# Optimization experiments

Hardware: AMD Instinct MI355X
Metric: run time of the kernel (lower is better)

## Reference

```python
import jax, jax.numpy as jnp
import numpy as np

B, S, D_MODEL, D_K, D_V, H = 2, 2048, 1024, 1024, 1024, 16


def setup_inputs() -> dict:
    key = jax.random.key(0)
    ks = jax.random.split(key, 12)
    s = 0.02
    inp = {
        "queries": jax.random.normal(ks[0], (B, S, D_MODEL), jnp.float32),
        "keys": jax.random.normal(ks[1], (B, S, D_MODEL), jnp.float32),
        "values": jax.random.normal(ks[2], (B, S, D_MODEL), jnp.float32),
        # causal mask: 1 where attention is disallowed (added as -1e9*mask)
        "mask": jnp.triu(jnp.ones((1, 1, S, S), jnp.float32), k=1),
        "Wq": jax.random.normal(ks[3], (D_MODEL, D_K), jnp.float32) * s,
        "bq": jnp.zeros((D_K,), jnp.float32),
        "Wk": jax.random.normal(ks[4], (D_MODEL, D_K), jnp.float32) * s,
        "bk": jnp.zeros((D_K,), jnp.float32),
        "Wv": jax.random.normal(ks[5], (D_MODEL, D_V), jnp.float32) * s,
        "bv": jnp.zeros((D_V,), jnp.float32),
        "Wo": jax.random.normal(ks[6], (D_K, D_MODEL), jnp.float32) * s,
        "bo": jnp.zeros((D_MODEL,), jnp.float32),
    }
    return inp


def _split_heads(x):  # [B,S,D] -> [B,H,S,D/H]
    b, s, d = x.shape
    return x.reshape(b, s, H, d // H).transpose(0, 2, 1, 3)


def reference(queries, keys, values, mask, Wq, bq, Wk, bk, Wv, bv, Wo, bo):
    q = _split_heads(queries @ Wq + bq)   # [B,H,S,hd]
    k = _split_heads(keys @ Wk + bk)
    v = _split_heads(values @ Wv + bv)
    # NOTE: original scales by sqrt(full d_k), not per-head dim (faithful quirk)
    scores = jnp.einsum("bhqd,bhkd->bhqk", q, k) / jnp.sqrt(jnp.float32(D_K))
    scores = scores + (-1e9) * mask
    w = jax.nn.softmax(scores, axis=-1)
    out = jnp.einsum("bhqk,bhkd->bhqd", w, v)        # [B,H,S,hd]
    out = out.transpose(0, 2, 1, 3).reshape(q.shape[0], q.shape[2], D_K)
    return out @ Wo + bo
```

## Files before the change

### kernel.cpp

```cpp
#include <hip/hip_runtime.h>
#include <hip/hip_bf16.h>
#include <cstdint>

typedef __bf16 bf16;
typedef __bf16 bf16x2 __attribute__((ext_vector_type(2)));
typedef __bf16 bf16x4 __attribute__((ext_vector_type(4)));
typedef __bf16 bf16x8 __attribute__((ext_vector_type(8)));
typedef float f32x4 __attribute__((ext_vector_type(4)));
typedef float f32x16 __attribute__((ext_vector_type(16)));
typedef unsigned int u32;

#define B_ 2
#define S_ 2048
#define DM 1024
#define H_ 16
#define HD 64

__device__ __forceinline__ void gload_lds16(const bf16* g, bf16* l) {
  __builtin_amdgcn_global_load_lds((const __attribute__((address_space(1))) void*)g,
                                   (__attribute__((address_space(3))) void*)l,
                                   16, 0, 0);
}

__device__ __forceinline__ u32 cvt_pk_bf16(float lo, float hi) {
  u32 r;
  asm("v_cvt_pk_bf16_f32 %0, %1, %2" : "=v"(r) : "v"(lo), "v"(hi));
  return r;
}

__device__ __forceinline__ bf16x8 cvt8(f32x4 lo, f32x4 hi) {
  bf16x8 o;
#pragma unroll
  for (int j = 0; j < 4; j++) { o[j] = (bf16)lo[j]; o[j + 4] = (bf16)hi[j]; }
  return o;
}

__global__ __launch_bounds__(256) void transposeW_k(
    const float* __restrict__ w0, const float* __restrict__ w1,
    const float* __restrict__ w2, const float* __restrict__ w3,
    bf16* __restrict__ t0, bf16* __restrict__ t1,
    bf16* __restrict__ t2, bf16* __restrict__ t3) {
  const float* src = (blockIdx.z == 0) ? w0 : (blockIdx.z == 1) ? w1
                     : (blockIdx.z == 2) ? w2 : w3;
  bf16* dst = (blockIdx.z == 0) ? t0 : (blockIdx.z == 1) ? t1
              : (blockIdx.z == 2) ? t2 : t3;
  __shared__ float tile[32][33];
  const int tx = threadIdx.x, ty = threadIdx.y;
  const int x0 = blockIdx.x * 32, y0 = blockIdx.y * 32;
#pragma unroll
  for (int r = 0; r < 4; r++)
    tile[ty + r * 8][tx] = src[(size_t)(y0 + ty + r * 8) * DM + x0 + tx];
  __syncthreads();
#pragma unroll
  for (int r = 0; r < 4; r++)
    dst[(size_t)(x0 + ty + r * 8) * DM + y0 + tx] = (bf16)tile[tx][ty + r * 8];
}

struct GArgs { const void* A; const bf16* Bt; const float* bias; void* C; };
struct GArgs3 { GArgs g[3]; };

__global__ __launch_bounds__(512, 1) void gemm128_k(GArgs3 args, int M, int N,
                                                    int K) {
  __shared__ __align__(16) bf16 SA_[73728];
  bf16* const SB_ = SA_ + 24576;

  const int nwg = gridDim.x;
  const int id = blockIdx.x;
  const int wgid = (id & 7) * (nwg >> 3) + (id >> 3);
  const int z = wgid >> 7;
  const int rem = wgid & 127;
  const int tx = rem & 3, ty = rem >> 2;
  const GArgs ga = args.g[z];
  const int m0 = ty * 128, n0 = tx * 256;

  const int tid = threadIdx.x;
  const int lane = tid & 63, w = tid >> 6;
  const int l15 = lane & 15, q = lane >> 4;
  const int wr = w >> 2, wc = w & 3;

  const float* gAf[2];
  int dAwr[2];
#pragma unroll
  for (int i = 0; i < 2; i++) {
    const int ci = i * 512 + w * 64 + lane;
    const int row = ci >> 3, sc = (ci & 7) ^ (row & 7);
    gAf[i] = (const float*)ga.A + (size_t)(m0 + row) * K + sc * 8;
    dAwr[i] = ci * 8;
  }
  const bf16* gB[4];
  int dB[4];
#pragma unroll
  for (int i = 0; i < 4; i++) {
    const int ci = i * 512 + w * 64 + lane;
    const int row = ci >> 3, sc = (ci & 7) ^ (row & 7);
    gB[i] = ga.Bt + (size_t)(n0 + row) * K + sc * 8;
    dB[i] = (i * 512 + w * 64) * 8;
  }

  const int cA0 = (q ^ (l15 & 7)) * 8;
  const int cA1 = ((4 + q) ^ (l15 & 7)) * 8;

  f32x4 acc[4][4] = {};
  const int NT = K >> 6;

  f32x4 a0l = *(const f32x4*)(gAf[0]);
  f32x4 a0h = *(const f32x4*)(gAf[0] + 4);
  f32x4 a1l = *(const f32x4*)(gAf[1]);
  f32x4 a1h = *(const f32x4*)(gAf[1] + 4);
  f32x4 c0l = *(const f32x4*)(gAf[0] + 64);
  f32x4 c0h = *(const f32x4*)(gAf[0] + 68);
  f32x4 c1l = *(const f32x4*)(gAf[1] + 64);
  f32x4 c1h = *(const f32x4*)(gAf[1] + 68);
#pragma unroll
  for (int i = 0; i < 4; i++) gload_lds16(gB[i], SB_ + dB[i]);
  f32x4 p0l = *(const f32x4*)(gAf[0] + 128);
  f32x4 p0h = *(const f32x4*)(gAf[0] + 132);
  f32x4 p1l = *(const f32x4*)(gAf[1] + 128);
  f32x4 p1h = *(const f32x4*)(gAf[1] + 132);
#pragma unroll
  for (int i = 0; i < 4; i++) gload_lds16(gB[i] + 64, SB_ + 16384 + dB[i]);
  *(bf16x8*)(SA_ + dAwr[0]) = cvt8(a0l, a0h);
  *(bf16x8*)(SA_ + dAwr[1]) = cvt8(a1l, a1h);
  *(bf16x8*)(SA_ + 8192 + dAwr[0]) = cvt8(c0l, c0h);
  *(bf16x8*)(SA_ + 8192 + dAwr[1]) = cvt8(c1l, c1h);
  asm volatile("s_waitcnt vmcnt(8) lgkmcnt(0)" ::: "memory");
  __builtin_amdgcn_s_barrier();

  for (int t = 0; t < NT; ++t) {
    const int rb = t % 3;
    const int w2 = (t + 2) % 3;
    *(bf16x8*)(SA_ + w2 * 8192 + dAwr[0]) = cvt8(p0l, p0h);
    *(bf16x8*)(SA_ + w2 * 8192 + dAwr[1]) = cvt8(p1l, p1h);
    const int ka = ((t + 3 < NT) ? t + 3 : NT - 1) << 6;
    p0l = *(const f32x4*)(gAf[0] + ka); p0h = *(const f32x4*)(gAf[0] + ka + 4);
    p1l = *(const f32x4*)(gAf[1] + ka); p1h = *(const f32x4*)(gAf[1] + ka + 4);
    const int kb2 = ((t + 2 < NT) ? t + 2 : NT - 1) << 6;
#pragma unroll
    for (int i = 0; i < 4; i++)
      gload_lds16(gB[i] + kb2, SB_ + w2 * 16384 + dB[i]);

    const bf16* Ab = SA_ + rb * 8192;
    const bf16* Bb = SB_ + rb * 16384;
    bf16x8 a[4][2], b[4][2];
#pragma unroll
    for (int mt = 0; mt < 4; mt++) {
      const int ro = (wr * 64 + mt * 16 + l15) * 64;
      a[mt][0] = *(const bf16x8*)(Ab + ro + cA0);
      a[mt][1] = *(const bf16x8*)(Ab + ro + cA1);
    }
#pragma unroll
    for (int nt = 0; nt < 4; nt++) {
      const int ro = (wc * 64 + nt * 16 + l15) * 64;
      b[nt][0] = *(const bf16x8*)(Bb + ro + cA0);
      b[nt][1] = *(const bf16x8*)(Bb + ro + cA1);
    }
    __builtin_amdgcn_s_setprio(1);
#pragma unroll
    for (int mt = 0; mt < 4; mt++)
#pragma unroll
      for (int nt = 0; nt < 4; nt++)
#pragma unroll
        for (int kk = 0; kk < 2; kk++)
          acc[mt][nt] = __builtin_amdgcn_mfma_f32_16x16x32_bf16(
              a[mt][kk], b[nt][kk], acc[mt][nt], 0, 0, 0);
    __builtin_amdgcn_s_setprio(0);

    asm volatile("s_waitcnt vmcnt(8) lgkmcnt(0)" ::: "memory");
    __builtin_amdgcn_s_barrier();
  }

  asm volatile("s_waitcnt vmcnt(0) lgkmcnt(0)" ::: "memory");
  __builtin_amdgcn_s_barrier();

  bf16* Ws = SA_ + w * 4352;
#pragma unroll
  for (int nt = 0; nt < 4; nt++) {
    const float bv = ga.bias[n0 + wc * 64 + nt * 16 + l15];
#pragma unroll
    for (int mt = 0; mt < 4; mt++)
#pragma unroll
      for (int r = 0; r < 4; r++)
        Ws[(mt * 16 + q * 4 + r) * 68 + nt * 16 + l15] =
            (bf16)(acc[mt][nt][r] + bv);
  }
#pragma unroll
  for (int p = 0; p < 8; p++) {
    const int lr = p * 8 + (lane >> 3), c0 = (lane & 7) * 8;
    bf16x4 lo = *(const bf16x4*)(Ws + lr * 68 + c0);
    bf16x4 hi = *(const bf16x4*)(Ws + lr * 68 + c0 + 4);
    bf16x8 o;
#pragma unroll
    for (int j = 0; j < 4; j++) { o[j] = lo[j]; o[j + 4] = hi[j]; }
    *(bf16x8*)((bf16*)ga.C + (size_t)(m0 + wr * 64 + lr) * N + n0 + wc * 64 + c0) = o;
  }
}

__global__ __launch_bounds__(512, 1) void gemmo_k(const bf16* __restrict__ A,
                                                  const bf16* __restrict__ Bt,
                                                  const float* __restrict__ bias,
                                                  float* __restrict__ C,
                                                  int M, int N, int K) {
  __shared__ __align__(16) bf16 SA_[49152];
  bf16* const SB_ = SA_ + 24576;

  const int id = blockIdx.x;
  const int wgid = (id & 7) * 32 + (id >> 3);
  const int tx = wgid & 7, ty = wgid >> 3;
  const int m0 = ty * 128, n0 = tx * 128;

  const int tid = threadIdx.x;
  const int lane = tid & 63, w = tid >> 6;
  const int l15 = lane & 15, q = lane >> 4;
  const int wr = w >> 2, wc = w & 3;

  const bf16* gA[2];
  const bf16* gB[2];
  int dd[2];
#pragma unroll
  for (int i = 0; i < 2; i++) {
    const int ci = i * 512 + w * 64 + lane;
    const int row = ci >> 3, sc = (ci & 7) ^ (row & 7);
    gA[i] = A + (size_t)(m0 + row) * K + sc * 8;
    gB[i] = Bt + (size_t)(n0 + row) * K + sc * 8;
    dd[i] = ci * 8;
  }

  const int cA0 = (q ^ (l15 & 7)) * 8;
  const int cA1 = ((4 + q) ^ (l15 & 7)) * 8;

  f32x4 acc[4][2] = {};
  const int NT = K >> 6;

#pragma unroll
  for (int tt = 0; tt < 2; tt++) {
    const int k0 = tt * 64;
    gload_lds16(gA[0] + k0, SA_ + tt * 8192 + dd[0]);
    gload_lds16(gA[1] + k0, SA_ + tt * 8192 + dd[1]);
    gload_lds16(gB[0] + k0, SB_ + tt * 8192 + dd[0]);
    gload_lds16(gB[1] + k0, SB_ + tt * 8192 + dd[1]);
  }
  asm volatile("s_waitcnt vmcnt(4)" ::: "memory");
  __builtin_amdgcn_s_barrier();

  for (int t = 0; t < NT; ++t) {
    const int rb = t % 3;
    const int wb = (t + 2) % 3;
    const int kpre = ((t + 2 < NT) ? t + 2 : NT - 1) << 6;
    gload_lds16(gA[0] + kpre, SA_ + wb * 8192 + dd[0]);
    gload_lds16(gA[1] + kpre, SA_ + wb * 8192 + dd[1]);
    gload_lds16(gB[0] + kpre, SB_ + wb * 8192 + dd[0]);
    gload_lds16(gB[1] + kpre, SB_ + wb * 8192 + dd[1]);

    const bf16* Ab = SA_ + rb * 8192;
    const bf16* Bb = SB_ + rb * 8192;
    bf16x8 a[4][2], b[2][2];
#pragma unroll
    for (int mt = 0; mt < 4; mt++) {
      const int ro = (wr * 64 + mt * 16 + l15) * 64;
      a[mt][0] = *(const bf16x8*)(Ab + ro + cA0);
      a[mt][1] = *(const bf16x8*)(Ab + ro + cA1);
    }
#pragma unroll
    for (int nt = 0; nt < 2; nt++) {
      const int ro = (wc * 32 + nt * 16 + l15) * 64;
      b[nt][0] = *(const bf16x8*)(Bb + ro + cA0);
      b[nt][1] = *(const bf16x8*)(Bb + ro + cA1);
    }

    __builtin_amdgcn_s_setprio(1);
#pragma unroll
    for (int mt = 0; mt < 4; mt++)
#pragma unroll
      for (int nt = 0; nt < 2; nt++)
#pragma unroll
        for (int kk = 0; kk < 2; kk++)
          acc[mt][nt] = __builtin_amdgcn_mfma_f32_16x16x32_bf16(
              a[mt][kk], b[nt][kk], acc[mt][nt], 0, 0, 0);
    __builtin_amdgcn_s_setprio(0);

    asm volatile("s_waitcnt vmcnt(4)" ::: "memory");
    __builtin_amdgcn_s_barrier();
  }

  asm volatile("s_waitcnt vmcnt(0)" ::: "memory");
  __builtin_amdgcn_s_barrier();

  float* Ws = (float*)SA_ + w * 2304;
#pragma unroll
  for (int nt = 0; nt < 2; nt++) {
    const float bv = bias[n0 + wc * 32 + nt * 16 + l15];
#pragma unroll
    for (int mt = 0; mt < 4; mt++)
#pragma unroll
      for (int r = 0; r < 4; r++)
        Ws[(mt * 16 + q * 4 + r) * 36 + nt * 16 + l15] = acc[mt][nt][r] + bv;
  }
#pragma unroll
  for (int p = 0; p < 8; p++) {
    const int lr = p * 8 + (lane >> 3), c0 = (lane & 7) * 4;
    f32x4 v = *(const f32x4*)(Ws + lr * 36 + c0);
    *(f32x4*)(C + (size_t)(m0 + wr * 64 + lr) * N + n0 + wc * 32 + c0) = v;
  }
}

__global__ __launch_bounds__(512, 4) void attn_k(const bf16* __restrict__ Qp,
                                                 const bf16* __restrict__ Kp,
                                                 const bf16* __restrict__ Vp,
                                                 bf16* __restrict__ Op) {
  const int g = blockIdx.x;
  const int xcd = g & 7, s = g >> 3;
  const int gl = s & 3, tau = s >> 2;
  const int bh = xcd * 4 + gl;
  const int b = bh >> 4, h = bh & 15;
  const int xt = (tau < 8) ? tau : 23 - tau;
  const int i0 = xt * 128;
  const int NI = 2 * xt + 2;

  const int tid = threadIdx.x;
  const int lane = tid & 63, w = tid >> 6;
  const int l31 = lane & 31, hi = lane >> 5;
  const int qq = w >> 1, kh = w & 1;

  __shared__ __align__(16) char smem[33792];
  bf16 (*Ks)[64][64] = (bf16 (*)[64][64])smem;
  bf16 (*Vts)[64][64] = (bf16 (*)[64][64])(smem + 16384);

  const size_t headoff = (size_t)b * S_ * DM + h * HD;
  const bf16* Kb = Kp + headoff;
  const bf16* Vb = Vp + headoff;

  const int kr = tid >> 3, kcb = (tid & 7) * 8;
  const int cK = ((tid & 7) ^ (kr & 7)) * 8;
  const int d0 = (tid & 31) * 2, kq = (tid >> 5) * 4;
  const int cV0 = ((kq >> 3) ^ (d0 & 7)) * 8 + (kq & 7);
  const int cV1 = ((kq >> 3) ^ ((d0 + 1) & 7)) * 8 + (kq & 7);
  const float QSCALE = 0.04508422f;

  bf16x8 qreg[4];
  {
    const bf16* qb = Qp + headoff + (size_t)(i0 + qq * 32 + l31) * DM + hi * 8;
#pragma unroll
    for (int kk = 0; kk < 4; kk++) {
      bf16x8 v = *(const bf16x8*)(qb + kk * 16);
      bf16x8 o;
#pragma unroll
      for (int j = 0; j < 8; j++) o[j] = (bf16)((float)v[j] * QSCALE);
      qreg[kk] = o;
    }
  }

  bf16x8 kR = *(const bf16x8*)(Kb + (size_t)kr * DM + kcb);
  bf16x2 vR[4];
#pragma unroll
  for (int j = 0; j < 4; j++)
    vR[j] = *(const bf16x2*)(Vb + (size_t)(kq + j) * DM + d0);
  *(bf16x8*)&Ks[0][kr][cK] = kR;
  {
    bf16x4 vlo, vhi;
#pragma unroll
    for (int j = 0; j < 4; j++) { vlo[j] = vR[j][0]; vhi[j] = vR[j][1]; }
    *(bf16x4*)&Vts[0][d0][cV0] = vlo;
    *(bf16x4*)&Vts[0][d0 + 1][cV1] = vhi;
  }
  kR = *(const bf16x8*)(Kb + (size_t)(64 + kr) * DM + kcb);
#pragma unroll
  for (int j = 0; j < 4; j++)
    vR[j] = *(const bf16x2*)(Vb + (size_t)(64 + kq + j) * DM + d0);
  __syncthreads();

  f32x16 oacc0 = {}, oacc1 = {};
  float rsum = 0.f;
  int buf = 0;
  const int qbase = i0 + qq * 32;

  for (int t = 0; t < NI; ++t, buf ^= 1) {
    if (t + 1 < NI) {
      *(bf16x8*)&Ks[buf ^ 1][kr][cK] = kR;
      bf16x4 vlo, vhi;
#pragma unroll
      for (int j = 0; j < 4; j++) { vlo[j] = vR[j][0]; vhi[j] = vR[j][1]; }
      *(bf16x4*)&Vts[buf ^ 1][d0][cV0] = vlo;
      *(bf16x4*)&Vts[buf ^ 1][d0 + 1][cV1] = vhi;
    }
    if (t + 2 < NI) {
      const size_t jn = (size_t)(t + 2) * 64;
      kR = *(const bf16x8*)(Kb + (jn + kr) * DM + kcb);
#pragma unroll
      for (int j = 0; j < 4; j++)
        vR[j] = *(const bf16x2*)(Vb + (jn + kq + j) * DM + d0);
    }

    const int kbase = t * 64 + kh * 32;
    if (kbase <= qbase + 31) {
      f32x16 sa = {}, sb = {};
      __builtin_amdgcn_s_setprio(1);
#pragma unroll
      for (int kk = 0; kk < 2; kk++) {
        bf16x8 ka = *(const bf16x8*)
            &Ks[buf][kh * 32 + l31][((2 * kk + hi) ^ (l31 & 7)) * 8];
        sa = __builtin_amdgcn_mfma_f32_32x32x16_bf16(ka, qreg[kk], sa, 0, 0, 0);
      }
#pragma unroll
      for (int kk = 2; kk < 4; kk++) {
        bf16x8 ka = *(const bf16x8*)
            &Ks[buf][kh * 32 + l31][((2 * kk + hi) ^ (l31 & 7)) * 8];
        sb = __builtin_amdgcn_mfma_f32_32x32x16_bf16(ka, qreg[kk], sb, 0, 0, 0);
      }
      __builtin_amdgcn_s_setprio(0);

      float p[16];
      if (kbase + 31 > qbase) {
        const int qrl = qbase + l31;
#pragma unroll
        for (int r = 0; r < 16; r++) {
          const int keyl = kbase + (r & 3) + 8 * (r >> 2) + 4 * hi;
          p[r] = (keyl <= qrl) ? __builtin_amdgcn_exp2f(sa[r] + sb[r]) : 0.f;
        }
      } else {
#pragma unroll
        for (int r = 0; r < 16; r++)
          p[r] = __builtin_amdgcn_exp2f(sa[r] + sb[r]);
      }
      {
        float q0 = (p[0] + p[1]) + (p[2] + p[3]);
        float q1 = (p[4] + p[5]) + (p[6] + p[7]);
        float q2 = (p[8] + p[9]) + (p[10] + p[11]);
        float q3 = (p[12] + p[13]) + (p[14] + p[15]);
        rsum += (q0 + q1) + (q2 + q3);
      }

      u32 Aq[4][2];
#pragma unroll
      for (int t2 = 0; t2 < 4; t2++) {
        Aq[t2][0] = cvt_pk_bf16(p[4 * t2 + 0], p[4 * t2 + 1]);
        Aq[t2][1] = cvt_pk_bf16(p[4 * t2 + 2], p[4 * t2 + 3]);
      }
      bf16x8 pb[2];
#pragma unroll
      for (int s2 = 0; s2 < 2; s2++) {
        auto e0 = __builtin_amdgcn_permlane32_swap(Aq[2 * s2][0], Aq[2 * s2 + 1][0], false, false);
        auto e1 = __builtin_amdgcn_permlane32_swap(Aq[2 * s2][1], Aq[2 * s2 + 1][1], false, false);
        union { u32 u[4]; bf16x8 v; } cv;
        cv.u[0] = e0[0]; cv.u[1] = e1[0]; cv.u[2] = e0[1]; cv.u[3] = e1[1];
        pb[s2] = cv.v;
      }

      __builtin_amdgcn_s_setprio(1);
#pragma unroll
      for (int s2 = 0; s2 < 2; s2++) {
        const int cv = ((kh * 4 + s2 * 2 + hi) ^ (l31 & 7)) * 8;
        bf16x8 va0 = *(const bf16x8*)&Vts[buf][l31][cv];
        bf16x8 va1 = *(const bf16x8*)&Vts[buf][32 + l31][cv];
        oacc0 = __builtin_amdgcn_mfma_f32_32x32x16_bf16(va0, pb[s2], oacc0, 0, 0, 0);
        oacc1 = __builtin_amdgcn_mfma_f32_32x32x16_bf16(va1, pb[s2], oacc1, 0, 0, 0);
      }
      __builtin_amdgcn_s_setprio(0);
    }

    __syncthreads();
  }

  float rtot_w = rsum + __shfl_xor(rsum, 32);
  float* osum = (float*)smem;
  float* auxf = (float*)(smem + 32768);
  if (kh == 0) {
#pragma unroll
    for (int m = 0; m < 2; m++)
#pragma unroll
      for (int rq = 0; rq < 4; rq++) {
        f32x4 v4;
#pragma unroll
        for (int e = 0; e < 4; e++)
          v4[e] = m ? oacc1[rq * 4 + e] : oacc0[rq * 4 + e];
        *(f32x4*)(osum + qq * 2048 + (m * 4 + rq) * 256 + lane * 4) = v4;
      }
  }
  if (lane < 32) auxf[w * 32 + lane] = rtot_w;
  __syncthreads();
  if (kh == 1) {
#pragma unroll
    for (int m = 0; m < 2; m++)
#pragma unroll
      for (int rq = 0; rq < 4; rq++) {
        float* pp = osum + qq * 2048 + (m * 4 + rq) * 256 + lane * 4;
        f32x4 v4 = *(f32x4*)pp;
#pragma unroll
        for (int e = 0; e < 4; e++)
          v4[e] += m ? oacc1[rq * 4 + e] : oacc0[rq * 4 + e];
        *(f32x4*)pp = v4;
      }
  }
  __syncthreads();

  {
    const int q = tid >> 2, q31b = q & 31, qq2 = q >> 5;
    const float rtot = auxf[(qq2 * 2 + 0) * 32 + q31b] + auxf[(qq2 * 2 + 1) * 32 + q31b];
    const float rinv = 1.0f / rtot;
    const int dbase = (tid & 3) * 16;
    bf16* orow = Op + headoff + (size_t)(i0 + q) * DM + dbase;
#pragma unroll
    for (int gg = 0; gg < 2; gg++) {
      bf16x8 o8;
#pragma unroll
      for (int e = 0; e < 8; e++) {
        const int d = dbase + gg * 8 + e;
        const int base = (((d >> 5) << 2) | ((d >> 3) & 3)) * 256 +
                         (q31b + 32 * ((d >> 2) & 1)) * 4 + (d & 3);
        o8[e] = (bf16)(osum[qq2 * 2048 + base] * rinv);
      }
      *(bf16x8*)(orow + gg * 8) = o8;
    }
  }
}

extern "C" void kernel_launch(void* const* d_in, const int* in_sizes, int n_in,
                              void* d_out, int out_size, void* d_ws, size_t ws_size,
                              hipStream_t stream) {
  const float* q_in = (const float*)d_in[0];
  const float* k_in = (const float*)d_in[1];
  const float* v_in = (const float*)d_in[2];
  const float* Wq = (const float*)d_in[4];
  const float* bq = (const float*)d_in[5];
  const float* Wk = (const float*)d_in[6];
  const float* bk = (const float*)d_in[7];
  const float* Wv = (const float*)d_in[8];
  const float* bv = (const float*)d_in[9];
  const float* Wo = (const float*)d_in[10];
  const float* bo = (const float*)d_in[11];

  bf16* ws = (bf16*)d_ws;
  const size_t NQ = (size_t)B_ * S_ * DM;
  bf16* Qp = ws;
  bf16* Kp = ws + NQ;
  bf16* Vp = ws + 2 * NQ;
  bf16* WqT = ws + 3 * NQ;
  bf16* WkT = WqT + (size_t)DM * DM;
  bf16* WvT = WkT + (size_t)DM * DM;
  bf16* WoT = WvT + (size_t)DM * DM;

  transposeW_k<<<dim3(32, 32, 4), dim3(32, 8), 0, stream>>>(
      Wq, Wk, Wv, Wo, WqT, WkT, WvT, WoT);

  GArgs3 g3;
  g3.g[0] = {q_in, WqT, bq, Qp};
  g3.g[1] = {k_in, WkT, bk, Kp};
  g3.g[2] = {v_in, WvT, bv, Vp};
  gemm128_k<<<dim3(384), 512, 0, stream>>>(g3, B_ * S_, DM, DM);

  attn_k<<<dim3(512, 1, 1), 512, 0, stream>>>(Qp, Kp, Vp, Qp);

  gemmo_k<<<dim3(256), 512, 0, stream>>>(Qp, WoT, bo, (float*)d_out,
                                         B_ * S_, DM, DM);
}
```

Baseline: 216.0 us.

## Deepen fp32 A-prefetch to two register sets and remap tile order in projection GEMM

The QKV projection GEMM now keeps two register sets of prefetched fp32 A tiles, loading A three to four k-steps ahead instead of three, and writes the converted tile to LDS after the MFMA block rather than before it. The loop is unrolled by two to alternate between the register sets, and the waitcnt threshold is raised to allow more loads in flight. The block-to-tile mapping is also switched to column-major (ty fastest), which changes L2 reuse of the B operand versus A. The goal is to hide global A-load latency behind compute, at the cost of extra VGPRs, and the loop now assumes NT is even.

```diff
diff --git a/kernel.cpp b/kernel.cpp
--- a/kernel.cpp
+++ b/kernel.cpp
@@ -69,7 +69,7 @@
   const int wgid = (id & 7) * (nwg >> 3) + (id >> 3);
   const int z = wgid >> 7;
   const int rem = wgid & 127;
-  const int tx = rem & 3, ty = rem >> 2;
+  const int tx = rem >> 5, ty = rem & 31;
   const GArgs ga = args.g[z];
   const int m0 = ty * 128, n0 = tx * 256;
 
@@ -113,60 +113,80 @@
   f32x4 c1h = *(const f32x4*)(gAf[1] + 68);
 #pragma unroll
   for (int i = 0; i < 4; i++) gload_lds16(gB[i], SB_ + dB[i]);
-  f32x4 p0l = *(const f32x4*)(gAf[0] + 128);
-  f32x4 p0h = *(const f32x4*)(gAf[0] + 132);
-  f32x4 p1l = *(const f32x4*)(gAf[1] + 128);
-  f32x4 p1h = *(const f32x4*)(gAf[1] + 132);
+  f32x4 A0_0l = *(const f32x4*)(gAf[0] + 128);
+  f32x4 A0_0h = *(const f32x4*)(gAf[0] + 132);
+  f32x4 A0_1l = *(const f32x4*)(gAf[1] + 128);
+  f32x4 A0_1h = *(const f32x4*)(gAf[1] + 132);
 #pragma unroll
   for (int i = 0; i < 4; i++) gload_lds16(gB[i] + 64, SB_ + 16384 + dB[i]);
+  f32x4 A1_0l = *(const f32x4*)(gAf[0] + 192);
+  f32x4 A1_0h = *(const f32x4*)(gAf[0] + 196);
+  f32x4 A1_1l = *(const f32x4*)(gAf[1] + 192);
+  f32x4 A1_1h = *(const f32x4*)(gAf[1] + 196);
   *(bf16x8*)(SA_ + dAwr[0]) = cvt8(a0l, a0h);
   *(bf16x8*)(SA_ + dAwr[1]) = cvt8(a1l, a1h);
   *(bf16x8*)(SA_ + 8192 + dAwr[0]) = cvt8(c0l, c0h);
   *(bf16x8*)(SA_ + 8192 + dAwr[1]) = cvt8(c1l, c1h);
-  asm volatile("s_waitcnt vmcnt(8) lgkmcnt(0)" ::: "memory");
+  asm volatile("s_waitcnt vmcnt(12) lgkmcnt(0)" ::: "memory");
   __builtin_amdgcn_s_barrier();
 
-  for (int t = 0; t < NT; ++t) {
-    const int rb = t % 3;
-    const int w2 = (t + 2) % 3;
-    *(bf16x8*)(SA_ + w2 * 8192 + dAwr[0]) = cvt8(p0l, p0h);
-    *(bf16x8*)(SA_ + w2 * 8192 + dAwr[1]) = cvt8(p1l, p1h);
-    const int ka = ((t + 3 < NT) ? t + 3 : NT - 1) << 6;
-    p0l = *(const f32x4*)(gAf[0] + ka); p0h = *(const f32x4*)(gAf[0] + ka + 4);
-    p1l = *(const f32x4*)(gAf[1] + ka); p1h = *(const f32x4*)(gAf[1] + ka + 4);
-    const int kb2 = ((t + 2 < NT) ? t + 2 : NT - 1) << 6;
-#pragma unroll
-    for (int i = 0; i < 4; i++)
-      gload_lds16(gB[i] + kb2, SB_ + w2 * 16384 + dB[i]);
-
-    const bf16* Ab = SA_ + rb * 8192;
-    const bf16* Bb = SB_ + rb * 16384;
-    bf16x8 a[4][2], b[4][2];
-#pragma unroll
-    for (int mt = 0; mt < 4; mt++) {
-      const int ro = (wr * 64 + mt * 16 + l15) * 64;
-      a[mt][0] = *(const bf16x8*)(Ab + ro + cA0);
-      a[mt][1] = *(const bf16x8*)(Ab + ro + cA1);
-    }
-#pragma unroll
-    for (int nt = 0; nt < 4; nt++) {
-      const int ro = (wc * 64 + nt * 16 + l15) * 64;
-      b[nt][0] = *(const bf16x8*)(Bb + ro + cA0);
-      b[nt][1] = *(const bf16x8*)(Bb + ro + cA1);
-    }
-    __builtin_amdgcn_s_setprio(1);
-#pragma unroll
-    for (int mt = 0; mt < 4; mt++)
-#pragma unroll
-      for (int nt = 0; nt < 4; nt++)
-#pragma unroll
-        for (int kk = 0; kk < 2; kk++)
-          acc[mt][nt] = __builtin_amdgcn_mfma_f32_16x16x32_bf16(
-              a[mt][kk], b[nt][kk], acc[mt][nt], 0, 0, 0);
-    __builtin_amdgcn_s_setprio(0);
-
-    asm volatile("s_waitcnt vmcnt(8) lgkmcnt(0)" ::: "memory");
-    __builtin_amdgcn_s_barrier();
+  for (int tt = 0; tt < NT; tt += 2) {
+#pragma unroll
+    for (int half = 0; half < 2; half++) {
+      const int t = tt + half;
+      const int rb = t % 3;
+      const int w2 = (t + 2) % 3;
+      const int kb2 = ((t + 2 < NT) ? t + 2 : NT - 1) << 6;
+#pragma unroll
+      for (int i = 0; i < 4; i++)
+        gload_lds16(gB[i] + kb2, SB_ + w2 * 16384 + dB[i]);
+
+      const bf16* Ab = SA_ + rb * 8192;
+      const bf16* Bb = SB_ + rb * 16384;
+      bf16x8 a[4][2], b[4][2];
+#pragma unroll
+      for (int mt = 0; mt < 4; mt++) {
+        const int ro = (wr * 64 + mt * 16 + l15) * 64;
+        a[mt][0] = *(const bf16x8*)(Ab + ro + cA0);
+        a[mt][1] = *(const bf16x8*)(Ab + ro + cA1);
+      }
+#pragma unroll
+      for (int nt = 0; nt < 4; nt++) {
+        const int ro = (wc * 64 + nt * 16 + l15) * 64;
+        b[nt][0] = *(const bf16x8*)(Bb + ro + cA0);
+        b[nt][1] = *(const bf16x8*)(Bb + ro + cA1);
+      }
+      __builtin_amdgcn_s_setprio(1);
+#pragma unroll
+      for (int mt = 0; mt < 4; mt++)
+#pragma unroll
+        for (int nt = 0; nt < 4; nt++)
+#pragma unroll
+          for (int kk = 0; kk < 2; kk++)
+            acc[mt][nt] = __builtin_amdgcn_mfma_f32_16x16x32_bf16(
+                a[mt][kk], b[nt][kk], acc[mt][nt], 0, 0, 0);
+      __builtin_amdgcn_s_setprio(0);
+
+      const int ka = ((t + 4 < NT) ? t + 4 : NT - 1) << 6;
+      if (half == 0) {
+        *(bf16x8*)(SA_ + w2 * 8192 + dAwr[0]) = cvt8(A0_0l, A0_0h);
+        *(bf16x8*)(SA_ + w2 * 8192 + dAwr[1]) = cvt8(A0_1l, A0_1h);
+        A0_0l = *(const f32x4*)(gAf[0] + ka);
+        A0_0h = *(const f32x4*)(gAf[0] + ka + 4);
+        A0_1l = *(const f32x4*)(gAf[1] + ka);
+        A0_1h = *(const f32x4*)(gAf[1] + ka + 4);
+      } else {
+        *(bf16x8*)(SA_ + w2 * 8192 + dAwr[0]) = cvt8(A1_0l, A1_0h);
+        *(bf16x8*)(SA_ + w2 * 8192 + dAwr[1]) = cvt8(A1_1l, A1_1h);
+        A1_0l = *(const f32x4*)(gAf[0] + ka);
+        A1_0h = *(const f32x4*)(gAf[0] + ka + 4);
+        A1_1l = *(const f32x4*)(gAf[1] + ka);
+        A1_1h = *(const f32x4*)(gAf[1] + ka + 4);
+      }
+
+      asm volatile("s_waitcnt vmcnt(12) lgkmcnt(0)" ::: "memory");
+      __builtin_amdgcn_s_barrier();
+    }
   }
 
   asm volatile("s_waitcnt vmcnt(0) lgkmcnt(0)" ::: "memory");
```

Measured after the change: 210.5 us. 2.5% less time.
